# Kernel optimization log

Measured on AMD Instinct MI355X. Metric: run time of the kernel, lower is better.

Reference implementation:

```python
import jax, jax.numpy as jnp
import numpy as np

EPS = 1e-6
N_HEAD, N_KV_HEAD = 16, 4
VE_GATE_CH = 12

def rmsnorm(x):
    return x * jax.lax.rsqrt(jnp.mean(x * x, axis=-1, keepdims=True) + EPS)

def apply_rotary_emb(x, cos, sin):
    half = x.shape[-1] // 2
    x1, x2 = x[..., :half], x[..., half:]
    return jnp.concatenate([x1 * cos + x2 * sin, -x1 * sin + x2 * cos], axis=-1)

def setup_inputs():
    key = jax.random.key(0)
    ks = jax.random.split(key, 8)
    B, S, D = 2, 2048, 1024
    H, KVH = N_HEAD, N_KV_HEAD
    hd = D // H
    x = jax.random.normal(ks[0], (B, S, D), jnp.float32)
    ve = jax.random.normal(ks[1], (B, S, KVH * hd), jnp.float32)
    # real rotary tables, broadcastable over [B,S,H,hd//2]
    inv_freq = 1.0 / (10000.0 ** (np.arange(hd // 2, dtype=np.float32) / (hd // 2)))
    ang = np.arange(S, dtype=np.float32)[:, None] * inv_freq[None, :]  # [S, hd//2]
    cos = jnp.asarray(np.cos(ang))[:, None, :]  # [S,1,hd//2]
    sin = jnp.asarray(np.sin(ang))[:, None, :]
    std = 0.02
    Wq = jax.random.normal(ks[2], (D, H * hd), jnp.float32) * std
    Wk = jax.random.normal(ks[3], (D, KVH * hd), jnp.float32) * std
    Wv = jax.random.normal(ks[4], (D, KVH * hd), jnp.float32) * std
    Wo = jax.random.normal(ks[5], (D, D), jnp.float32) * std
    Wg = jax.random.normal(ks[6], (VE_GATE_CH, KVH), jnp.float32) * std
    return {"x": x, "ve": ve, "cos": cos, "sin": sin, "Wq": Wq, "Wk": Wk,
            "Wv": Wv, "Wo": Wo, "Wg": Wg, "window_size": 512}

def reference(x, ve, cos, sin, Wq, Wk, Wv, Wo, Wg, window_size):
    B, S, D = x.shape
    H, KVH = N_HEAD, N_KV_HEAD
    hd = D // H
    q = (x @ Wq).reshape(B, S, H, hd)
    k = (x @ Wk).reshape(B, S, KVH, hd)
    v = (x @ Wv).reshape(B, S, KVH, hd)
    # value-embedding gating
    gate = 3.0 * jax.nn.sigmoid(x[..., :VE_GATE_CH] @ Wg)  # [B,S,KVH]
    v = v + gate[..., None] * ve.reshape(B, S, KVH, hd)
    # RoPE + QK rmsnorm * 1.2
    q = rmsnorm(apply_rotary_emb(q, cos, sin)) * 1.2
    k = rmsnorm(apply_rotary_emb(k, cos, sin)) * 1.2
    # GQA head repeat (repeat_interleave over head dim)
    rep = H // KVH
    k = jnp.repeat(k, rep, axis=2)  # [B,S,H,hd]
    v = jnp.repeat(v, rep, axis=2)
    scale = 1.0 / np.sqrt(hd).astype(np.float32)
    scores = jnp.einsum('bqhd,bkhd->bhqk', q, k) * scale  # [B,H,S,S]
    pos = jnp.arange(S)
    allow = (pos[None, :] <= pos[:, None]) & (pos[None, :] >= pos[:, None] - window_size + 1)
    scores = jnp.where(allow[None, None], scores, -jnp.inf)
    attn = jax.nn.softmax(scores, axis=-1)
    y = jnp.einsum('bhqk,bkhd->bqhd', attn, v).reshape(B, S, D)
    return y @ Wo
```

## Files before the change

kernel.cpp:

```cpp
#include <hip/hip_runtime.h>
#include <hip/hip_bf16.h>
#include <cstddef>
#include <cstdint>


typedef short v8s __attribute__((ext_vector_type(8)));
typedef float v4f __attribute__((ext_vector_type(4)));

__device__ __forceinline__ ushort b1(float a) {
  uint u = __float_as_uint(a);
  return (ushort)((u + 0x7FFFu + ((u >> 16) & 1u)) >> 16);
}
__device__ __forceinline__ uint bpack(float lo, float hi) {
  uint ul = __float_as_uint(lo), uh = __float_as_uint(hi);
  ul = (ul + 0x7FFFu + ((ul >> 16) & 1u)) >> 16;
  uh = (uh + 0x7FFFu + ((uh >> 16) & 1u)) & 0xFFFF0000u;
  return ul | uh;
}

__device__ __forceinline__ void async16(const ushort* g, ushort* l) {
  __builtin_amdgcn_global_load_lds(
      (__attribute__((address_space(1))) void*)(uintptr_t)(const void*)g,
      (__attribute__((address_space(3))) void*)(uintptr_t)(void*)l, 16, 0, 0);
}

__global__ __launch_bounds__(256) void prep_all(
    const float* __restrict__ x, ushort* __restrict__ xb,
    const float* __restrict__ Wg, float* __restrict__ gates,
    const float* __restrict__ cosp, const float* __restrict__ sinp,
    float2* __restrict__ cs,
    const float* __restrict__ Wq, const float* __restrict__ Wk,
    const float* __restrict__ Wv, const float* __restrict__ Wo,
    ushort* __restrict__ Wqt, ushort* __restrict__ Wkt,
    ushort* __restrict__ Wvt, ushort* __restrict__ Wot)
{
  const int bx = blockIdx.x, t = threadIdx.x;
  if (bx < 4096) {
    const float* row = x + (size_t)bx * 1024;
    float4 v = *(const float4*)(row + t * 4);
    ushort4 o;
    o.x = b1(v.x); o.y = b1(v.y); o.z = b1(v.z); o.w = b1(v.w);
    *(ushort4*)(xb + (size_t)bx * 1024 + t * 4) = o;
    if (t < 4) {
      float g = 0.f;
#pragma unroll
      for (int i = 0; i < 12; ++i) g += row[i] * Wg[i * 4 + t];
      gates[bx * 4 + t] = 3.0f / (1.0f + __expf(-g));
    }
    return;
  }
  if (bx < 4352) {
    const int i = (bx - 4096) * 256 + t;
    cs[i] = make_float2(cosp[i], sinp[i]);
    return;
  }
  __shared__ ushort tile[32][33];
  int u = bx - 4352;
  const float* W; ushort* Wt; int N, xx, yy;
  if (u < 1024)      { W = Wq; Wt = Wqt; N = 1024; xx = u & 31; yy = u >> 5; }
  else if (u < 2048) { u -= 1024; W = Wo; Wt = Wot; N = 1024; xx = u & 31; yy = u >> 5; }
  else if (u < 2304) { u -= 2048; W = Wk; Wt = Wkt; N = 256;  xx = u & 7;  yy = u >> 3; }
  else               { u -= 2304; W = Wv; Wt = Wvt; N = 256;  xx = u & 7;  yy = u >> 3; }
  const int n0 = xx * 32, k0 = yy * 32;
  const int tx = t & 31, ty = t >> 5;
#pragma unroll
  for (int i = 0; i < 4; ++i) {
    const int k = ty + i * 8;
    tile[k][tx] = b1(W[(size_t)(k0 + k) * N + n0 + tx]);
  }
  __syncthreads();
#pragma unroll
  for (int i = 0; i < 4; ++i) {
    const int n = ty + i * 8;
    Wt[(size_t)(n0 + n) * 1024 + k0 + tx] = tile[tx][n];
  }
}

__device__ __forceinline__ void gemm_mainloop(
    const ushort* __restrict__ A, const ushort* __restrict__ Bt,
    int K, int m0, int n0, ushort (*As)[64], ushort (*Bs)[64],
    v4f acc[4][4])
{
  const int t = threadIdx.x;
  const int lane = t & 63, wave = t >> 6;
  const int wr = wave >> 1, wc = wave & 1;
  const int quad = lane >> 4, l16 = lane & 15;
  const int l8 = lane >> 3, c8 = (lane & 7) * 8;

  const ushort* ap[4];
  const ushort* bp[4];
  ushort* al[4];
  ushort* bl[4];
#pragma unroll
  for (int i = 0; i < 4; ++i) {
    const int row = (wave * 4 + i) * 8 + l8;
    ap[i] = A  + (size_t)(m0 + row) * K + c8;
    bp[i] = Bt + (size_t)(n0 + row) * K + c8;
    al[i] = &As[(wave * 4 + i) * 8][0];
    bl[i] = &Bs[(wave * 4 + i) * 8][0];
  }

  for (int k0 = 0; k0 < K; k0 += 64) {
#pragma unroll
    for (int i = 0; i < 4; ++i) {
      async16(ap[i] + k0, al[i]);
      async16(bp[i] + k0, bl[i]);
    }
    __syncthreads();
#pragma unroll
    for (int ks = 0; ks < 2; ++ks) {
      v8s af[4], bf[4];
#pragma unroll
      for (int i = 0; i < 4; ++i) {
        af[i] = *(const v8s*)&As[wr * 64 + i * 16 + l16][ks * 32 + quad * 8];
        bf[i] = *(const v8s*)&Bs[wc * 64 + i * 16 + l16][ks * 32 + quad * 8];
      }
#pragma unroll
      for (int mt = 0; mt < 4; ++mt)
#pragma unroll
        for (int nt = 0; nt < 4; ++nt)
          acc[mt][nt] = __builtin_amdgcn_mfma_f32_16x16x32_bf16(
              af[mt], bf[nt], acc[mt][nt], 0, 0, 0);
    }
    __syncthreads();
  }
}

__global__ __launch_bounds__(256) void gemm_qkv_fused(
    const ushort* __restrict__ A, const ushort* __restrict__ Bt,
    const float2* __restrict__ cs, const float* __restrict__ gates,
    const float* __restrict__ ve,
    ushort* __restrict__ qb, ushort* __restrict__ kb, ushort* __restrict__ vb)
{
  __shared__ ushort As[128][64];
  __shared__ ushort Bs[128][64];
  const int m0 = blockIdx.x * 128, n0 = blockIdx.y * 128;
  const int lane = threadIdx.x & 63, wave = threadIdx.x >> 6;
  const int wr = wave >> 1, wc = wave & 1;
  const int quad = lane >> 4, l16 = lane & 15;

  v4f acc[4][4];
#pragma unroll
  for (int i = 0; i < 4; ++i)
#pragma unroll
    for (int j = 0; j < 4; ++j) acc[i][j] = (v4f){0.f, 0.f, 0.f, 0.f};

  gemm_mainloop(A, Bt, 1024, m0, n0, As, Bs, acc);

  const int sec = blockIdx.y;
  const int head_col = n0 + wc * 64;

  if (sec < 10) {
    const bool isQ = (sec < 8);
    const int h = (head_col - (isQ ? 0 : 1024)) >> 6;
    ushort* dst = isQ ? qb : kb;
    const int ld = isQ ? 1024 : 256;
#pragma unroll
    for (int mt = 0; mt < 4; ++mt)
#pragma unroll
      for (int r = 0; r < 4; ++r) {
        const int row = m0 + wr * 64 + mt * 16 + quad * 4 + r;
        const int s = row & 2047;
        const float2 cs0 = cs[s * 32 + l16];
        const float2 cs1 = cs[s * 32 + 16 + l16];
        const float x10 = acc[mt][0][r], x11 = acc[mt][1][r];
        const float x20 = acc[mt][2][r], x21 = acc[mt][3][r];
        float ss = x10 * x10 + x11 * x11 + x20 * x20 + x21 * x21;
        ss += __shfl_xor(ss, 1);
        ss += __shfl_xor(ss, 2);
        ss += __shfl_xor(ss, 4);
        ss += __shfl_xor(ss, 8);
        const float rs = rsqrtf(ss * (1.0f / 64.0f) + 1e-6f) * 1.2f;
        ushort* dp = dst + (size_t)row * ld + h * 64 + l16;
        dp[0]  = b1((x10 * cs0.x + x20 * cs0.y) * rs);
        dp[16] = b1((x11 * cs1.x + x21 * cs1.y) * rs);
        dp[32] = b1((-x10 * cs0.y + x20 * cs0.x) * rs);
        dp[48] = b1((-x11 * cs1.y + x21 * cs1.x) * rs);
      }
  } else {
    const int kvh = (head_col - 1280) >> 6;
#pragma unroll
    for (int mt = 0; mt < 4; ++mt)
#pragma unroll
      for (int r = 0; r < 4; ++r) {
        const int row = m0 + wr * 64 + mt * 16 + quad * 4 + r;
        const float gate = gates[row * 4 + kvh];
        const float* vep = ve + (size_t)row * 256 + kvh * 64 + l16;
        ushort* dp = vb + (size_t)row * 256 + kvh * 64 + l16;
#pragma unroll
        for (int nt = 0; nt < 4; ++nt)
          dp[nt * 16] = b1(acc[mt][nt][r] + gate * vep[nt * 16]);
      }
  }
}

__global__ __launch_bounds__(256) void gemm_wo(
    const ushort* __restrict__ A, const ushort* __restrict__ Bt,
    float* __restrict__ C)
{
  __shared__ ushort As[128][64];
  __shared__ ushort Bs[128][64];
  const int m0 = blockIdx.x * 128, n0 = blockIdx.y * 128;
  const int lane = threadIdx.x & 63, wave = threadIdx.x >> 6;
  const int wr = wave >> 1, wc = wave & 1;
  const int quad = lane >> 4, l16 = lane & 15;

  v4f acc[4][4];
#pragma unroll
  for (int i = 0; i < 4; ++i)
#pragma unroll
    for (int j = 0; j < 4; ++j) acc[i][j] = (v4f){0.f, 0.f, 0.f, 0.f};

  gemm_mainloop(A, Bt, 1024, m0, n0, As, Bs, acc);

#pragma unroll
  for (int mt = 0; mt < 4; ++mt)
#pragma unroll
    for (int r = 0; r < 4; ++r) {
      float* cp = C + (size_t)(m0 + wr * 64 + mt * 16 + quad * 4 + r) * 1024
                    + n0 + wc * 64 + l16;
#pragma unroll
      for (int nt = 0; nt < 4; ++nt) cp[nt * 16] = acc[mt][nt][r];
    }
}

__global__ __launch_bounds__(256) void transpose_v(
    const ushort* __restrict__ vb, ushort* __restrict__ vtb)
{
  __shared__ ushort L[64][72];
  const int s0 = blockIdx.x * 64, kvh = blockIdx.y, b = blockIdx.z;
  const int t = threadIdx.x;
#pragma unroll
  for (int i = 0; i < 2; ++i) {
    const int cc = t + i * 256;
    const int srow = cc >> 3, c8 = (cc & 7) * 8;
    *(int4*)&L[srow][c8] =
        *(const int4*)(vb + ((size_t)(b * 2048 + s0 + srow)) * 256 + kvh * 64 + c8);
  }
  __syncthreads();
#pragma unroll
  for (int i = 0; i < 2; ++i) {
    const int cc = t + i * 256;
    const int drow = cc >> 3, s8 = (cc & 7) * 8;
    ushort w[8];
#pragma unroll
    for (int jj = 0; jj < 8; ++jj) w[jj] = L[s8 + jj][drow];
    *(int4*)(vtb + ((size_t)((b * 4 + kvh) * 64 + drow)) * 2048 + s0 + s8) =
        *(int4*)w;
  }
}

__global__ __launch_bounds__(256) void attn_mfma(
    const ushort* __restrict__ qb, const ushort* __restrict__ kb,
    const ushort* __restrict__ vtb, ushort* __restrict__ yb,
    const int* __restrict__ wptr)
{
  __shared__ ushort Ks[64][72];
  __shared__ ushort Vt[80][72];
  __shared__ ushort Ps[128][72];
  const int qt = blockIdx.x, h = blockIdx.y, b = blockIdx.z;
  const int kvh = h >> 2, q0 = qt * 128;
  const int t = threadIdx.x, lane = t & 63, wave = t >> 6;
  const int quad = lane >> 4, l16 = lane & 15;
  const int Wwin = *wptr;

  v8s qf[2][2];
#pragma unroll
  for (int s = 0; s < 2; ++s) {
    const ushort* qp = qb + ((size_t)(b * 2048 + q0 + wave * 32 + s * 16 + l16)) * 1024
                          + h * 64 + quad * 8;
    qf[s][0] = *(const v8s*)qp;
    qf[s][1] = *(const v8s*)(qp + 32);
  }

  if (t < 128) {
    const int row = 64 + (t >> 3), c8 = (t & 7) * 8;
    const int v = (row == 64) ? 0x3F803F80 : 0;
    int4 w; w.x = v; w.y = v; w.z = v; w.w = v;
    *(int4*)&Vt[row][c8] = w;
  }

  v4f o[2][5];
#pragma unroll
  for (int s = 0; s < 2; ++s)
#pragma unroll
    for (int d = 0; d < 5; ++d) o[s][d] = (v4f){0.f, 0.f, 0.f, 0.f};

  const int lo = q0 - Wwin + 1;
  const int kt0 = (lo > 0) ? (lo >> 6) : 0;
  const int kt1 = (q0 + 127) >> 6;

  for (int kt = kt0; kt <= kt1; ++kt) {
#pragma unroll
    for (int i = 0; i < 2; ++i) {
      const int cc = t + i * 256;
      const int r8 = cc >> 3, c8 = (cc & 7) * 8;
      *(int4*)&Ks[r8][c8] =
          *(const int4*)(kb + ((size_t)(b * 2048 + kt * 64 + r8)) * 256 + kvh * 64 + c8);
      *(int4*)&Vt[r8][c8] =
          *(const int4*)(vtb + ((size_t)((b * 4 + kvh) * 64 + r8)) * 2048 + kt * 64 + c8);
    }
    __syncthreads();

    const bool needs_mask = (kt * 64 + 63 > q0) || (kt * 64 < q0 + 128 - Wwin);

#pragma unroll
    for (int s = 0; s < 2; ++s) {
      const int qrow = q0 + wave * 32 + s * 16 + l16;
      ushort* prow = &Ps[wave * 32 + s * 16 + l16][0];
#pragma unroll
      for (int nt = 0; nt < 4; ++nt) {
        v8s kf0 = *(const v8s*)&Ks[nt * 16 + l16][quad * 8];
        v8s kf1 = *(const v8s*)&Ks[nt * 16 + l16][32 + quad * 8];
        v4f st = (v4f){0.f, 0.f, 0.f, 0.f};
        st = __builtin_amdgcn_mfma_f32_16x16x32_bf16(kf0, qf[s][0], st, 0, 0, 0);
        st = __builtin_amdgcn_mfma_f32_16x16x32_bf16(kf1, qf[s][1], st, 0, 0, 0);
        float p[4];
#pragma unroll
        for (int r = 0; r < 4; ++r) {
          p[r] = exp2f(fmaf(st[r], 0.18033688011f, -17.31234049107f));
          if (needs_mask) {
            const int k = kt * 64 + nt * 16 + quad * 4 + r;
            const bool ok = (k <= qrow) && (k > qrow - Wwin);
            p[r] = ok ? p[r] : 0.0f;
          }
        }
        uint2 w;
        w.x = bpack(p[0], p[1]);
        w.y = bpack(p[2], p[3]);
        *(uint2*)(prow + nt * 16 + quad * 4) = w;
      }
    }

    v8s pf[2][2];
#pragma unroll
    for (int s = 0; s < 2; ++s) {
      pf[s][0] = *(const v8s*)&Ps[wave * 32 + s * 16 + l16][quad * 8];
      pf[s][1] = *(const v8s*)&Ps[wave * 32 + s * 16 + l16][32 + quad * 8];
    }
#pragma unroll
    for (int dt = 0; dt < 5; ++dt) {
      v8s vf0 = *(const v8s*)&Vt[dt * 16 + l16][quad * 8];
      v8s vf1 = *(const v8s*)&Vt[dt * 16 + l16][32 + quad * 8];
#pragma unroll
      for (int s = 0; s < 2; ++s) {
        o[s][dt] = __builtin_amdgcn_mfma_f32_16x16x32_bf16(pf[s][0], vf0, o[s][dt], 0, 0, 0);
        o[s][dt] = __builtin_amdgcn_mfma_f32_16x16x32_bf16(pf[s][1], vf1, o[s][dt], 0, 0, 0);
      }
    }
    __syncthreads();
  }

#pragma unroll
  for (int s = 0; s < 2; ++s)
#pragma unroll
    for (int r = 0; r < 4; ++r) {
      const float l = __shfl(o[s][4][r], lane & 48);
      const float inv = 1.0f / l;
      ushort* yp = yb + ((size_t)(b * 2048 + q0 + wave * 32 + s * 16 + quad * 4 + r)) * 1024
                      + h * 64 + l16;
#pragma unroll
      for (int dt = 0; dt < 4; ++dt) yp[dt * 16] = b1(o[s][dt][r] * inv);
    }
}

extern "C" void kernel_launch(void* const* d_in, const int* in_sizes, int n_in,
                              void* d_out, int out_size, void* d_ws, size_t ws_size,
                              hipStream_t stream)
{
  const float* x    = (const float*)d_in[0];
  const float* ve   = (const float*)d_in[1];
  const float* cosp = (const float*)d_in[2];
  const float* sinp = (const float*)d_in[3];
  const float* Wq   = (const float*)d_in[4];
  const float* Wk   = (const float*)d_in[5];
  const float* Wv   = (const float*)d_in[6];
  const float* Wo   = (const float*)d_in[7];
  const float* Wg   = (const float*)d_in[8];
  const int*   win  = (const int*)d_in[9];
  float* out = (float*)d_out;

  char* p = (char*)d_ws;
  ushort* xb    = (ushort*)p;  p += (size_t)4194304 * 2;
  ushort* qb    = (ushort*)p;  p += (size_t)4194304 * 2;
  ushort* yb    = (ushort*)p;  p += (size_t)4194304 * 2;
  ushort* kb    = (ushort*)p;  p += (size_t)1048576 * 2;
  ushort* vb    = (ushort*)p;  p += (size_t)1048576 * 2;
  ushort* vtb   = (ushort*)p;  p += (size_t)1048576 * 2;
  ushort* Wqkvt = (ushort*)p;  p += (size_t)1536 * 1024 * 2;
  ushort* Wot   = (ushort*)p;  p += (size_t)1048576 * 2;
  float2* cs    = (float2*)p;  p += (size_t)65536 * 8;
  float*  gates = (float*)p;

  prep_all<<<6912, 256, 0, stream>>>(
      x, xb, Wg, gates, cosp, sinp, cs, Wq, Wk, Wv, Wo,
      Wqkvt, Wqkvt + (size_t)1024 * 1024, Wqkvt + (size_t)1280 * 1024, Wot);

  gemm_qkv_fused<<<dim3(32, 12), 256, 0, stream>>>(xb, Wqkvt, cs, gates, ve,
                                                   qb, kb, vb);
  transpose_v<<<dim3(32, 4, 2), 256, 0, stream>>>(vb, vtb);

  attn_mfma<<<dim3(16, 16, 2), 256, 0, stream>>>(qb, kb, vtb, yb, win);

  gemm_wo<<<dim3(32, 8), 256, 0, stream>>>(yb, Wot, out);
}
```

Measured before the change: 176.4 us.

## Fuse V transpose into QKV epilogue and double-buffer K/V tiles in attention

```diff
diff --git a/kernel.cpp b/kernel.cpp
--- a/kernel.cpp
+++ b/kernel.cpp
@@ -10,12 +10,6 @@
 __device__ __forceinline__ ushort b1(float a) {
   uint u = __float_as_uint(a);
   return (ushort)((u + 0x7FFFu + ((u >> 16) & 1u)) >> 16);
-}
-__device__ __forceinline__ uint bpack(float lo, float hi) {
-  uint ul = __float_as_uint(lo), uh = __float_as_uint(hi);
-  ul = (ul + 0x7FFFu + ((ul >> 16) & 1u)) >> 16;
-  uh = (uh + 0x7FFFu + ((uh >> 16) & 1u)) & 0xFFFF0000u;
-  return ul | uh;
 }
 
 __device__ __forceinline__ void async16(const ushort* g, ushort* l) {
@@ -130,7 +124,7 @@
     const ushort* __restrict__ A, const ushort* __restrict__ Bt,
     const float2* __restrict__ cs, const float* __restrict__ gates,
     const float* __restrict__ ve,
-    ushort* __restrict__ qb, ushort* __restrict__ kb, ushort* __restrict__ vb)
+    ushort* __restrict__ qb, ushort* __restrict__ kb, ushort* __restrict__ vtb)
 {
   __shared__ ushort As[128][64];
   __shared__ ushort Bs[128][64];
@@ -180,17 +174,28 @@
   } else {
     const int kvh = (head_col - 1280) >> 6;
 #pragma unroll
-    for (int mt = 0; mt < 4; ++mt)
+    for (int mt = 0; mt < 4; ++mt) {
+      const int row0 = m0 + wr * 64 + mt * 16 + quad * 4;
+      const int bb = row0 >> 11;
+      const int s0 = row0 & 2047;
+      float pv[4][4];
 #pragma unroll
       for (int r = 0; r < 4; ++r) {
-        const int row = m0 + wr * 64 + mt * 16 + quad * 4 + r;
+        const int row = row0 + r;
         const float gate = gates[row * 4 + kvh];
         const float* vep = ve + (size_t)row * 256 + kvh * 64 + l16;
-        ushort* dp = vb + (size_t)row * 256 + kvh * 64 + l16;
 #pragma unroll
         for (int nt = 0; nt < 4; ++nt)
-          dp[nt * 16] = b1(acc[mt][nt][r] + gate * vep[nt * 16]);
-      }
+          pv[nt][r] = acc[mt][nt][r] + gate * vep[nt * 16];
+      }
+#pragma unroll
+      for (int nt = 0; nt < 4; ++nt) {
+        ushort4 w;
+        w.x = b1(pv[nt][0]); w.y = b1(pv[nt][1]);
+        w.z = b1(pv[nt][2]); w.w = b1(pv[nt][3]);
+        *(ushort4*)(vtb + ((size_t)((bb * 4 + kvh) * 64 + nt * 16 + l16)) * 2048 + s0) = w;
+      }
+    }
   }
 }
 
@@ -224,39 +229,13 @@
     }
 }
 
-__global__ __launch_bounds__(256) void transpose_v(
-    const ushort* __restrict__ vb, ushort* __restrict__ vtb)
-{
-  __shared__ ushort L[64][72];
-  const int s0 = blockIdx.x * 64, kvh = blockIdx.y, b = blockIdx.z;
-  const int t = threadIdx.x;
-#pragma unroll
-  for (int i = 0; i < 2; ++i) {
-    const int cc = t + i * 256;
-    const int srow = cc >> 3, c8 = (cc & 7) * 8;
-    *(int4*)&L[srow][c8] =
-        *(const int4*)(vb + ((size_t)(b * 2048 + s0 + srow)) * 256 + kvh * 64 + c8);
-  }
-  __syncthreads();
-#pragma unroll
-  for (int i = 0; i < 2; ++i) {
-    const int cc = t + i * 256;
-    const int drow = cc >> 3, s8 = (cc & 7) * 8;
-    ushort w[8];
-#pragma unroll
-    for (int jj = 0; jj < 8; ++jj) w[jj] = L[s8 + jj][drow];
-    *(int4*)(vtb + ((size_t)((b * 4 + kvh) * 64 + drow)) * 2048 + s0 + s8) =
-        *(int4*)w;
-  }
-}
-
 __global__ __launch_bounds__(256) void attn_mfma(
     const ushort* __restrict__ qb, const ushort* __restrict__ kb,
     const ushort* __restrict__ vtb, ushort* __restrict__ yb,
     const int* __restrict__ wptr)
 {
-  __shared__ ushort Ks[64][72];
-  __shared__ ushort Vt[80][72];
+  __shared__ ushort Ks[2][64][72];
+  __shared__ ushort Vt[2][80][72];
   __shared__ ushort Ps[128][72];
   const int qt = blockIdx.x, h = blockIdx.y, b = blockIdx.z;
   const int kvh = h >> 2, q0 = qt * 128;
@@ -274,10 +253,11 @@
   }
 
   if (t < 128) {
-    const int row = 64 + (t >> 3), c8 = (t & 7) * 8;
+    const int row = 64 + (t >> 3), cc8 = (t & 7) * 8;
     const int v = (row == 64) ? 0x3F803F80 : 0;
     int4 w; w.x = v; w.y = v; w.z = v; w.w = v;
-    *(int4*)&Vt[row][c8] = w;
+    *(int4*)&Vt[0][row][cc8] = w;
+    *(int4*)&Vt[1][row][cc8] = w;
   }
 
   v4f o[2][5];
@@ -290,17 +270,33 @@
   const int kt0 = (lo > 0) ? (lo >> 6) : 0;
   const int kt1 = (q0 + 127) >> 6;
 
+  const int r8 = t >> 3, c8s = (t & 7) * 8;
+  const ushort* kbase = kb + ((size_t)(b * 2048 + r8)) * 256 + kvh * 64 + c8s;
+  const ushort* vbase = vtb + ((size_t)((b * 4 + kvh) * 64 + r8)) * 2048 + c8s;
+
+  int4 kr[2], vr[2];
+#pragma unroll
+  for (int i = 0; i < 2; ++i) {
+    kr[i] = *(const int4*)(kbase + (size_t)(kt0 * 64 + i * 32) * 256);
+    vr[i] = *(const int4*)(vbase + (size_t)(i * 32) * 2048 + kt0 * 64);
+  }
+
   for (int kt = kt0; kt <= kt1; ++kt) {
+    const int pb = kt & 1;
 #pragma unroll
     for (int i = 0; i < 2; ++i) {
-      const int cc = t + i * 256;
-      const int r8 = cc >> 3, c8 = (cc & 7) * 8;
-      *(int4*)&Ks[r8][c8] =
-          *(const int4*)(kb + ((size_t)(b * 2048 + kt * 64 + r8)) * 256 + kvh * 64 + c8);
-      *(int4*)&Vt[r8][c8] =
-          *(const int4*)(vtb + ((size_t)((b * 4 + kvh) * 64 + r8)) * 2048 + kt * 64 + c8);
+      *(int4*)&Ks[pb][r8 + i * 32][c8s] = kr[i];
+      *(int4*)&Vt[pb][r8 + i * 32][c8s] = vr[i];
     }
     __syncthreads();
+
+    if (kt < kt1) {
+#pragma unroll
+      for (int i = 0; i < 2; ++i) {
+        kr[i] = *(const int4*)(kbase + (size_t)((kt + 1) * 64 + i * 32) * 256);
+        vr[i] = *(const int4*)(vbase + (size_t)(i * 32) * 2048 + (kt + 1) * 64);
+      }
+    }
 
     const bool needs_mask = (kt * 64 + 63 > q0) || (kt * 64 < q0 + 128 - Wwin);
 
@@ -310,11 +306,13 @@
       ushort* prow = &Ps[wave * 32 + s * 16 + l16][0];
 #pragma unroll
       for (int nt = 0; nt < 4; ++nt) {
-        v8s kf0 = *(const v8s*)&Ks[nt * 16 + l16][quad * 8];
-        v8s kf1 = *(const v8s*)&Ks[nt * 16 + l16][32 + quad * 8];
+        v8s kf0 = *(const v8s*)&Ks[pb][nt * 16 + l16][quad * 8];
+        v8s kf1 = *(const v8s*)&Ks[pb][nt * 16 + l16][32 + quad * 8];
         v4f st = (v4f){0.f, 0.f, 0.f, 0.f};
+        __builtin_amdgcn_s_setprio(1);
         st = __builtin_amdgcn_mfma_f32_16x16x32_bf16(kf0, qf[s][0], st, 0, 0, 0);
         st = __builtin_amdgcn_mfma_f32_16x16x32_bf16(kf1, qf[s][1], st, 0, 0, 0);
+        __builtin_amdgcn_s_setprio(0);
         float p[4];
 #pragma unroll
         for (int r = 0; r < 4; ++r) {
@@ -326,8 +324,8 @@
           }
         }
         uint2 w;
-        w.x = bpack(p[0], p[1]);
-        w.y = bpack(p[2], p[3]);
+        asm("v_cvt_pk_bf16_f32 %0, %1, %2" : "=v"(w.x) : "v"(p[0]), "v"(p[1]));
+        asm("v_cvt_pk_bf16_f32 %0, %1, %2" : "=v"(w.y) : "v"(p[2]), "v"(p[3]));
         *(uint2*)(prow + nt * 16 + quad * 4) = w;
       }
     }
@@ -340,15 +338,16 @@
     }
 #pragma unroll
     for (int dt = 0; dt < 5; ++dt) {
-      v8s vf0 = *(const v8s*)&Vt[dt * 16 + l16][quad * 8];
-      v8s vf1 = *(const v8s*)&Vt[dt * 16 + l16][32 + quad * 8];
+      v8s vf0 = *(const v8s*)&Vt[pb][dt * 16 + l16][quad * 8];
+      v8s vf1 = *(const v8s*)&Vt[pb][dt * 16 + l16][32 + quad * 8];
+      __builtin_amdgcn_s_setprio(1);
 #pragma unroll
       for (int s = 0; s < 2; ++s) {
         o[s][dt] = __builtin_amdgcn_mfma_f32_16x16x32_bf16(pf[s][0], vf0, o[s][dt], 0, 0, 0);
         o[s][dt] = __builtin_amdgcn_mfma_f32_16x16x32_bf16(pf[s][1], vf1, o[s][dt], 0, 0, 0);
       }
-    }
-    __syncthreads();
+      __builtin_amdgcn_s_setprio(0);
+    }
   }
 
 #pragma unroll
@@ -385,7 +384,6 @@
   ushort* qb    = (ushort*)p;  p += (size_t)4194304 * 2;
   ushort* yb    = (ushort*)p;  p += (size_t)4194304 * 2;
   ushort* kb    = (ushort*)p;  p += (size_t)1048576 * 2;
-  ushort* vb    = (ushort*)p;  p += (size_t)1048576 * 2;
   ushort* vtb   = (ushort*)p;  p += (size_t)1048576 * 2;
   ushort* Wqkvt = (ushort*)p;  p += (size_t)1536 * 1024 * 2;
   ushort* Wot   = (ushort*)p;  p += (size_t)1048576 * 2;
@@ -397,8 +395,7 @@
       Wqkvt, Wqkvt + (size_t)1024 * 1024, Wqkvt + (size_t)1280 * 1024, Wot);
 
   gemm_qkv_fused<<<dim3(32, 12), 256, 0, stream>>>(xb, Wqkvt, cs, gates, ve,
-                                                   qb, kb, vb);
-  transpose_v<<<dim3(32, 4, 2), 256, 0, stream>>>(vb, vtb);
+                                                   qb, kb, vtb);
 
   attn_mfma<<<dim3(16, 16, 2), 256, 0, stream>>>(qb, kb, vtb, yb, win);
 
```

New measurement: 217.6 us. 23.4% more time.
